# Performance work log

Measured on AMD Instinct MI355X. Metric: run time of the kernel, lower is better.

## Reference

```python
import math
import jax, jax.numpy as jnp
import numpy as np

B, N, C, H = 64, 197, 768, 12
KEEP_RATE = 0.7

def setup_inputs() -> dict:
    key = jax.random.key(0)
    k0, k1, k2 = jax.random.split(key, 3)
    x = jax.random.normal(k0, (B, N, C), jnp.float32)
    qkv_w = jax.random.normal(k1, (C, 3 * C), jnp.float32) * 0.02
    qkv_b = jnp.zeros((3 * C,), jnp.float32)
    proj_w = jax.random.normal(k2, (C, C), jnp.float32) * 0.02
    proj_b = jnp.zeros((C,), jnp.float32)
    return {"x": x, "qkv_w": qkv_w, "qkv_b": qkv_b, "proj_w": proj_w, "proj_b": proj_b}

def reference(x, qkv_w, qkv_b, proj_w, proj_b):
    b, n, c = x.shape
    d = c // H
    scale = d ** -0.5
    # qkv: [B,N,3C] -> [3,B,H,N,d]
    qkv = (x @ qkv_w + qkv_b).reshape(b, n, 3, H, d)
    qkv = jnp.transpose(qkv, (2, 0, 3, 1, 4))
    q, k, v = qkv[0], qkv[1], qkv[2]
    attn = jax.nn.softmax(jnp.einsum('bhnd,bhmd->bhnm', q, k) * scale, axis=-1)  # [B,H,N,N]
    out = jnp.einsum('bhnm,bhmd->bhnd', attn, v)          # [B,H,N,d]
    out = jnp.transpose(out, (0, 2, 1, 3)).reshape(b, n, c)
    x_out = out @ proj_w + proj_b                          # [B,N,C]
    # dynamic token pruning via CLS attention (row 0, excluding CLS itself)
    left_tokens = math.ceil(KEEP_RATE * (n - 1))
    cls_attn = attn[:, :, 0, 1:].mean(axis=1)              # [B,N-1]
    _, idx = jax.lax.top_k(cls_attn, left_tokens)          # descending, sorted
    index = jnp.broadcast_to(idx[:, :, None], (b, left_tokens, c))
    return (x_out, index, idx, cls_attn, left_tokens)
```

## Files before the change

### kernel.cpp

```cpp
#include <hip/hip_runtime.h>
#include <math.h>

#define BB   64
#define NTOK 197
#define CC   768
#define HH   12
#define DH   64
#define MTOT (BB * NTOK)
#define MPAD 12672
#define LEFT 138

#define XOUT_OFF  0
#define INDEX_OFF 9682944
#define IDX_OFF   16465920
#define CLS_OFF   16474752
#define LT_OFF    16487296

typedef short s8v __attribute__((ext_vector_type(8)));
typedef short s4v __attribute__((ext_vector_type(4)));
typedef float f4v __attribute__((ext_vector_type(4)));

#define GLOAD16(g, l) __builtin_amdgcn_global_load_lds( \
    (const __attribute__((address_space(1))) unsigned int*)(g), \
    (__attribute__((address_space(3))) unsigned int*)(l), 16, 0, 0)

__device__ __forceinline__ unsigned short f2bf(float f) {
    union { float f; unsigned int i; } x; x.f = f;
    unsigned int r = x.i + 0x7FFFu + ((x.i >> 16) & 1u);
    return (unsigned short)(r >> 16);
}


__device__ __forceinline__ void convert_x_body(int blk, int tid,
        const float* __restrict__ in, unsigned short* __restrict__ outb)
{
    size_t i = ((size_t)blk * 256 + tid) * 8;
    float4 a = *(const float4*)(in + i);
    float4 b = *(const float4*)(in + i + 4);
    s8v r;
    r[0] = (short)f2bf(a.x); r[1] = (short)f2bf(a.y);
    r[2] = (short)f2bf(a.z); r[3] = (short)f2bf(a.w);
    r[4] = (short)f2bf(b.x); r[5] = (short)f2bf(b.y);
    r[6] = (short)f2bf(b.z); r[7] = (short)f2bf(b.w);
    *(s8v*)(outb + i) = r;
}

__device__ __forceinline__ void transpose_w_body(int q, int tid, char* smem,
        const float* __restrict__ inq, const float* __restrict__ inp,
        unsigned short* __restrict__ outq, unsigned short* __restrict__ outp)
{
    float (*tile)[33] = (float(*)[33])smem;
    const int bi = q % 24;
    int bj = q / 24;
    const float* in; unsigned short* outb; int N;
    if (bj < 72) { in = inq; outb = outq; N = 2304; }
    else         { bj -= 72; in = inp; outb = outp; N = 768; }
    const int tx = tid & 31, ty = tid >> 5;
#pragma unroll
    for (int r = ty; r < 32; r += 8)
        tile[r][tx] = in[(size_t)(bi * 32 + r) * N + bj * 32 + tx];
    __syncthreads();
#pragma unroll
    for (int r = ty; r < 32; r += 8)
        outb[(size_t)(bj * 32 + r) * 768 + bi * 32 + tx] = f2bf(tile[tx][r]);
}

#define QCH  64
#define BGRP 8
__device__ __forceinline__ void qr96_body(int q, int tid, char* smem,
        const float* __restrict__ x, const float* __restrict__ qkv_w,
        const float* __restrict__ qkv_b, float* __restrict__ rws,
        float* __restrict__ bconst)
{
    const int h  = q % HH;
    const int b0 = (q / HH) * BGRP;
    float (*x0s)[CC] = (float(*)[CC])smem;
    float* wbuf0 = (float*)(smem + 24576);
    float* wbuf1 = (float*)(smem + 40960);
    float (*q0s)[DH] = (float(*)[DH])(smem + 57344);

    for (int u = tid; u < BGRP * CC; u += 256) {
        int b = u / CC, c = u - b * CC;
        x0s[b][c] = x[(size_t)(b0 + b) * NTOK * CC + c];
    }
    for (int u = tid; u < QCH * DH; u += 256) {
        int cc = u >> 6, dd = u & 63;
        wbuf0[u] = qkv_w[(size_t)cc * 2304 + h * DH + dd];
    }
    __syncthreads();

    const int d  = tid & 63;
    const int bA = tid >> 6;
    const int bB = bA + 4;
    float accA = qkv_b[h * DH + d];
    float accB = qkv_b[h * DH + d];
    for (int k = 0; k < CC / QCH; ++k) {
        float* wcur  = (k & 1) ? wbuf1 : wbuf0;
        float* wnext = (k & 1) ? wbuf0 : wbuf1;
        if (k + 1 < CC / QCH) {
            const int cbase = (k + 1) * QCH;
            for (int u = tid; u < QCH * DH; u += 256) {
                int cc = u >> 6, dd = u & 63;
                wnext[u] = qkv_w[(size_t)(cbase + cc) * 2304 + h * DH + dd];
            }
        }
        const int cb = k * QCH;
#pragma unroll
        for (int cc = 0; cc < QCH; ++cc) {
            const float wv = wcur[cc * 64 + d];
            accA = fmaf(x0s[bA][cb + cc], wv, accA);
            accB = fmaf(x0s[bB][cb + cc], wv, accB);
        }
        __syncthreads();
    }
    q0s[bA][d] = accA;
    q0s[bB][d] = accB;
    __syncthreads();

    if (tid < BGRP) {
        float acc3 = 0.f;
        for (int dd = 0; dd < DH; ++dd) acc3 += q0s[tid][dd] * qkv_b[CC + h * DH + dd];
        bconst[(b0 + tid) * HH + h] = acc3;
    }

    for (int c = tid; c < CC; c += 256) {
        const float* wrow = qkv_w + (size_t)c * 2304 + CC + h * DH;
        float acc2[BGRP];
#pragma unroll
        for (int b = 0; b < BGRP; ++b) acc2[b] = 0.f;
#pragma unroll
        for (int dd = 0; dd < DH; dd += 4) {
            float4 w4 = *(const float4*)(wrow + dd);
#pragma unroll
            for (int b = 0; b < BGRP; ++b) {
                acc2[b] = fmaf(w4.x, q0s[b][dd + 0], acc2[b]);
                acc2[b] = fmaf(w4.y, q0s[b][dd + 1], acc2[b]);
                acc2[b] = fmaf(w4.z, q0s[b][dd + 2], acc2[b]);
                acc2[b] = fmaf(w4.w, q0s[b][dd + 3], acc2[b]);
            }
        }
#pragma unroll
        for (int b = 0; b < BGRP; ++b)
            rws[((size_t)(b0 + b) * HH + h) * CC + c] = acc2[b];
    }
}

__device__ __forceinline__ void gemm_body(int id, int tid, char* smem,
        const unsigned short* __restrict__ A, const unsigned short* __restrict__ BT,
        const float* __restrict__ bias, int ncolt, int mode,
        unsigned short* __restrict__ outb, float* __restrict__ outf)
{
    const int xcd = id & 7;
    const int t = id >> 3;
    const int ct = t % ncolt, s = t / ncolt;
    const int rt = s * 8 + xcd;
    if (rt >= 99) return;
    const int m0 = rt * 128, n0 = ct * 128;

    const int wave = tid >> 6, lane = tid & 63;
    const int quad = lane >> 4, l16 = lane & 15;
    const int rowbase = (wave >> 1) * 64, colbase = (wave & 1) * 64;
    short* As = (short*)smem;
    short* Bs = (short*)(smem + 16384);

    const int rA   = lane >> 3;
    const int gcol = ((lane & 7) ^ rA) * 8;
    unsigned int agof[4], bgof[4];
#pragma unroll
    for (int i = 0; i < 4; ++i) {
        int c = wave * 4 + i;
        agof[i] = (unsigned int)((m0 + c * 8 + rA) * 768 + gcol);
        bgof[i] = (unsigned int)((n0 + c * 8 + rA) * 768 + gcol);
    }
    int aoff[4], boff[4];
#pragma unroll
    for (int i = 0; i < 4; ++i) {
        aoff[i] = (rowbase + i * 16 + l16) * 64 + ((quad ^ (l16 & 7)) * 8);
        boff[i] = (colbase + i * 16 + l16) * 64 + ((quad ^ (l16 & 7)) * 8);
    }

    f4v acc[4][4];
#pragma unroll
    for (int i = 0; i < 4; ++i)
#pragma unroll
        for (int j = 0; j < 4; ++j) acc[i][j] = (f4v)0.f;

    for (int k0 = 0; k0 < 768; k0 += 64) {
#pragma unroll
        for (int i = 0; i < 4; ++i) {
            int c = wave * 4 + i;
            GLOAD16(A  + agof[i] + k0, &As[c * 512]);
            GLOAD16(BT + bgof[i] + k0, &Bs[c * 512]);
        }
        __syncthreads();
#pragma unroll
        for (int ks = 0; ks < 2; ++ks) {
            const int x = ks * 32;
            s8v af[4], bf[4];
#pragma unroll
            for (int i = 0; i < 4; ++i) af[i] = *(const s8v*)&As[aoff[i] ^ x];
#pragma unroll
            for (int j = 0; j < 4; ++j) bf[j] = *(const s8v*)&Bs[boff[j] ^ x];
#pragma unroll
            for (int i = 0; i < 4; ++i)
#pragma unroll
                for (int j = 0; j < 4; ++j)
                    acc[i][j] = __builtin_amdgcn_mfma_f32_16x16x32_bf16(bf[j], af[i], acc[i][j], 0, 0, 0);
        }
        __syncthreads();
    }

    const int ncols = mode ? 768 : 2304;
#pragma unroll
    for (int i = 0; i < 4; ++i) {
        const int m = m0 + rowbase + i * 16 + l16;
        if (m >= MTOT) continue;
#pragma unroll
        for (int j = 0; j < 4; ++j) {
            const int nb = n0 + colbase + j * 16 + quad * 4;
            float4 b4 = *(const float4*)&bias[nb];
            if (mode == 1) {
                float4 r;
                r.x = acc[i][j][0] + b4.x; r.y = acc[i][j][1] + b4.y;
                r.z = acc[i][j][2] + b4.z; r.w = acc[i][j][3] + b4.w;
                *(float4*)(outf + (size_t)m * ncols + nb) = r;
            } else {
                s4v r;
                r[0] = (short)f2bf(acc[i][j][0] + b4.x);
                r[1] = (short)f2bf(acc[i][j][1] + b4.y);
                r[2] = (short)f2bf(acc[i][j][2] + b4.z);
                r[3] = (short)f2bf(acc[i][j][3] + b4.w);
                *(s4v*)(outb + (size_t)m * ncols + nb) = r;
            }
        }
    }
}

__device__ __forceinline__ void cls_s_body(int q, int tid, char* smem,
        const float* __restrict__ x, const float* __restrict__ rws,
        const float* __restrict__ bconst, float* __restrict__ sws)
{
    const int bx = q % 10, b = q / 10;
    float* rl  = (float*)smem;
    float* bcs = (float*)(smem + 37056);
#pragma unroll
    for (int h = 0; h < HH; ++h)
        for (int c = tid; c < CC; c += 256)
            rl[h * 772 + c] = rws[((size_t)b * HH + h) * CC + c];
    if (tid < HH) bcs[tid] = bconst[b * HH + tid];
    __syncthreads();
    const int local = bx * 256 + tid;
    if (local < NTOK * HH) {
        const int tok = local / HH;
        const int h = local - tok * HH;
        const float* xr = x + ((size_t)b * NTOK + tok) * CC;
        const float* rp = rl + h * 772;
        float acc = 0.f;
#pragma unroll 8
        for (int c = 0; c < CC; c += 4) {
            float4 x4 = *(const float4*)(xr + c);
            float4 r4 = *(const float4*)(rp + c);
            acc = fmaf(x4.x, r4.x, acc);
            acc = fmaf(x4.y, r4.y, acc);
            acc = fmaf(x4.z, r4.z, acc);
            acc = fmaf(x4.w, r4.w, acc);
        }
        sws[((size_t)b * HH + h) * NTOK + tok] = (acc + bcs[h]) * 0.125f;
    }
}

#define VTS 224
__device__ __forceinline__ void transpose_v_body(int q, int tid, char* smem,
        const unsigned short* __restrict__ qkv, unsigned short* __restrict__ vt)
{
    short (*tile)[33] = (short(*)[33])smem;
    const int bx = q % 7;
    const int by = (q / 7) & 1;
    const int bh = q / 14;
    const int b = bh / HH, h = bh - b * HH;
    const int tx = tid & 31, ty = tid >> 5;
    const unsigned short* vin = qkv + (size_t)b * NTOK * 2304 + 1536 + h * DH;
#pragma unroll
    for (int r = ty; r < 32; r += 8) {
        const int tok = bx * 32 + r;
        tile[r][tx] = (tok < NTOK) ? (short)vin[(size_t)tok * 2304 + by * 32 + tx] : (short)0;
    }
    __syncthreads();
#pragma unroll
    for (int r = ty; r < 32; r += 8) {
        const int d = by * 32 + r;
        vt[((size_t)bh * DH + d) * VTS + bx * 32 + tx] = tile[tx][r];
    }
}

__device__ __forceinline__ void cls_topk_body(int b, int tid, char* smem,
        const float* __restrict__ sws, float* __restrict__ out, int write_lt)
{
    const int wave = tid >> 6, lane = tid & 63;
    float (*sbuf)[208] = (float(*)[208])smem;
    float (*pm)[208]   = (float(*)[208])(smem + 9984);
    float* vals        = (float*)(smem + 13312);
    int*   idxs        = (int*)(smem + 14336);

    for (int jj = lane; jj < 208; jj += 64) pm[wave][jj] = 0.f;
    if (tid < NTOK) {
#pragma unroll
        for (int h = 0; h < HH; ++h)
            sbuf[h][tid] = sws[((size_t)b * HH + h) * NTOK + tid];
    }
    __syncthreads();

    for (int h = wave; h < HH; h += 4) {
        float sv[4], ev[4];
        float mx = -1e30f;
#pragma unroll
        for (int t = 0; t < 4; ++t) {
            int j = lane + 64 * t;
            sv[t] = (j < NTOK) ? sbuf[h][j] : -1e30f;
            mx = fmaxf(mx, sv[t]);
        }
#pragma unroll
        for (int off = 1; off < 64; off <<= 1) mx = fmaxf(mx, __shfl_xor(mx, off, 64));
        float sm = 0.f;
#pragma unroll
        for (int t = 0; t < 4; ++t) {
            int j = lane + 64 * t;
            ev[t] = (j < NTOK) ? expf(sv[t] - mx) : 0.f;
            sm += ev[t];
        }
#pragma unroll
        for (int off = 1; off < 64; off <<= 1) sm += __shfl_xor(sm, off, 64);
#pragma unroll
        for (int t = 0; t < 4; ++t) {
            int j = lane + 64 * t;
            if (j < NTOK) pm[wave][j] += ev[t] / sm;
        }
    }
    __syncthreads();

    float v = -INFINITY;
    int id = 256 + tid;
    if (tid < NTOK - 1) {
        int j = tid + 1;
        float s = ((pm[0][j] + pm[1][j]) + (pm[2][j] + pm[3][j])) * (1.f / 12.f);
        v = s; id = tid;
        out[CLS_OFF + (size_t)b * (NTOK - 1) + tid] = s;
    }
    vals[tid] = v; idxs[tid] = id;
    __syncthreads();

    for (int k = 2; k <= 256; k <<= 1) {
        for (int j = k >> 1; j > 0; j >>= 1) {
            int ixj = tid ^ j;
            if (ixj > tid) {
                float va = vals[tid], vb2 = vals[ixj];
                int ia = idxs[tid], ib = idxs[ixj];
                bool aLess = (va > vb2) || (va == vb2 && ia < ib);
                bool dir = ((tid & k) == 0);
                if (dir != aLess) {
                    vals[tid] = vb2; vals[ixj] = va;
                    idxs[tid] = ib;  idxs[ixj] = ia;
                }
            }
            __syncthreads();
        }
    }

    if (tid < LEFT) out[IDX_OFF + (size_t)b * LEFT + tid] = (float)idxs[tid];
    if (write_lt && b == 0 && tid == 0) out[LT_OFF] = (float)LEFT;
}

__device__ __forceinline__ void write_index_body(int row, int tid,
        const float* __restrict__ idx_in, float* __restrict__ out)
{
    const float v = idx_in[row];
    if (tid < 192) {
        float4 r; r.x = v; r.y = v; r.z = v; r.w = v;
        *(float4*)(out + INDEX_OFF + (size_t)row * CC + tid * 4) = r;
    }
}

#define PSTR 226
__device__ __forceinline__ void attn_body(int bh, int g, int tid,
        short* Ks, short* Ps,
        const unsigned short* __restrict__ qkv, const unsigned short* __restrict__ vt,
        unsigned short* __restrict__ attnbf)
{
    const int b = bh / HH, h = bh - b * HH;
    const int wave = tid >> 6, lane = tid & 63;
    const int quad = lane >> 4, l16 = lane & 15;

    const unsigned short* qg = qkv + (size_t)b * NTOK * 2304 + h * DH;
    const unsigned short* kg = qg + 768;
    const unsigned short* vtb = vt + (size_t)bh * DH * VTS;

    for (int u = tid; u < NTOK * 8; u += 256) {
        const int row = u >> 3, seg = u & 7;
        *(s8v*)&Ks[row * 64 + (seg ^ (row & 7)) * 8] =
            *(const s8v*)(kg + (size_t)row * 2304 + seg * 8);
    }
    __syncthreads();

    const int strip = g * 4 + wave;
    if (strip >= 13) return;

    const int mq = min(strip * 16 + l16, NTOK - 1);
    const s8v aq0 = *(const s8v*)(qg + (size_t)mq * 2304 + quad * 8);
    const s8v aq1 = *(const s8v*)(qg + (size_t)mq * 2304 + 32 + quad * 8);

    f4v sacc[14];
#pragma unroll
    for (int j = 0; j < 14; ++j) sacc[j] = (f4v)0.f;
    __builtin_amdgcn_s_setprio(1);
#pragma unroll
    for (int j = 0; j < 14; ++j) {
        const int kt = min(j * 16 + l16, NTOK - 1);
        s8v bk0 = *(const s8v*)&Ks[kt * 64 + ((quad       ^ (kt & 7)) * 8)];
        s8v bk1 = *(const s8v*)&Ks[kt * 64 + (((quad + 4) ^ (kt & 7)) * 8)];
        sacc[j] = __builtin_amdgcn_mfma_f32_16x16x32_bf16(bk0, aq0, sacc[j], 0, 0, 0);
        sacc[j] = __builtin_amdgcn_mfma_f32_16x16x32_bf16(bk1, aq1, sacc[j], 0, 0, 0);
    }
    __builtin_amdgcn_s_setprio(0);

    s8v bvr[7][4];
#pragma unroll
    for (int t = 0; t < 7; ++t) {
        const int ko = t * 32 + quad * 8;
#pragma unroll
        for (int j = 0; j < 4; ++j)
            bvr[t][j] = *(const s8v*)(vtb + (size_t)(j * 16 + l16) * VTS + ko);
    }

    float mx = -1e30f;
#pragma unroll
    for (int j = 0; j < 14; ++j)
#pragma unroll
        for (int r = 0; r < 4; ++r) {
            const int key = j * 16 + quad * 4 + r;
            float s = (key < NTOK) ? sacc[j][r] * 0.125f : -1e30f;
            sacc[j][r] = s;
            mx = fmaxf(mx, s);
        }
    mx = fmaxf(mx, __shfl_xor(mx, 16, 64));
    mx = fmaxf(mx, __shfl_xor(mx, 32, 64));

    float sm = 0.f;
#pragma unroll
    for (int j = 0; j < 14; ++j) {
        s4v pk;
#pragma unroll
        for (int r = 0; r < 4; ++r) {
            const int key = j * 16 + quad * 4 + r;
            float p = (key < NTOK) ? __expf(sacc[j][r] - mx) : 0.f;
            sm += p;
            pk[r] = (short)f2bf(p);
        }
        *(s4v*)&Ps[wave * 16 * PSTR + l16 * PSTR + j * 16 + quad * 4] = pk;
    }
    sm += __shfl_xor(sm, 16, 64);
    sm += __shfl_xor(sm, 32, 64);
    const float rcp = 1.f / sm;

    f4v oacc[4];
#pragma unroll
    for (int j = 0; j < 4; ++j) oacc[j] = (f4v)0.f;
    __builtin_amdgcn_s_setprio(1);
#pragma unroll
    for (int t = 0; t < 7; ++t) {
        const int ko = t * 32 + quad * 8;
        s8v ap = *(const s8v*)&Ps[wave * 16 * PSTR + l16 * PSTR + ko];
#pragma unroll
        for (int j = 0; j < 4; ++j)
            oacc[j] = __builtin_amdgcn_mfma_f32_16x16x32_bf16(bvr[t][j], ap, oacc[j], 0, 0, 0);
    }
    __builtin_amdgcn_s_setprio(0);
    const int qrow = strip * 16 + l16;
    if (qrow < NTOK) {
#pragma unroll
        for (int j = 0; j < 4; ++j) {
            s4v o4;
#pragma unroll
            for (int r = 0; r < 4; ++r) o4[r] = (short)f2bf(oacc[j][r] * rcp);
            *(s4v*)&attnbf[((size_t)b * NTOK + qrow) * 768 + h * DH + j * 16 + quad * 4] = o4;
        }
    }
}

#define PRE_QR 96
#define PRE_CV 4728
#define PRE_TW 2304

__global__ __launch_bounds__(256)
void fat_pre(const float* __restrict__ x, const float* __restrict__ qkv_w,
             const float* __restrict__ qkv_b, const float* __restrict__ proj_w,
             unsigned short* __restrict__ xbf, unsigned short* __restrict__ wt1,
             unsigned short* __restrict__ wt2, float* __restrict__ rws,
             float* __restrict__ bconst)
{
    __shared__ __align__(16) char smem[59392];
    const int id = blockIdx.x, tid = threadIdx.x;
    if (id < PRE_QR)
        qr96_body(id, tid, smem, x, qkv_w, qkv_b, rws, bconst);
    else if (id < PRE_QR + PRE_CV)
        convert_x_body(id - PRE_QR, tid, x, xbf);
    else
        transpose_w_body(id - PRE_QR - PRE_CV, tid, smem, qkv_w, proj_w, wt1, wt2);
}

#define QKV_GEMM (8 * 18 * 13)

__global__ __launch_bounds__(256, 3)
void fat_qkv(const unsigned short* __restrict__ xbf, const unsigned short* __restrict__ wt1,
             const float* __restrict__ qkv_b, unsigned short* __restrict__ qkvbf,
             const float* __restrict__ x, const float* __restrict__ rws,
             const float* __restrict__ bconst, float* __restrict__ sws)
{
    __shared__ __align__(16) char smem[37104];
    const int id = blockIdx.x, tid = threadIdx.x;
    if (id < QKV_GEMM)
        gemm_body(id, tid, smem, xbf, wt1, qkv_b, 18, 0, qkvbf, nullptr);
    else
        cls_s_body(id - QKV_GEMM, tid, smem, x, rws, bconst, sws);
}

__global__ __launch_bounds__(256)
void fat_tv(const unsigned short* __restrict__ qkvbf, unsigned short* __restrict__ vt,
            const float* __restrict__ sws, float* __restrict__ out, int write_lt)
{
    __shared__ __align__(16) char smem[15360];
    const int id = blockIdx.x, tid = threadIdx.x;
    if (id < 64)
        cls_topk_body(id, tid, smem, sws, out, write_lt);
    else
        transpose_v_body(id - 64, tid, smem, qkvbf, vt);
}

#define ATTN_BLKS (768 * 4)

__global__ __launch_bounds__(256, 2)
void fat_attn(const unsigned short* __restrict__ qkv, const unsigned short* __restrict__ vt,
              unsigned short* __restrict__ attnbf,
              const float* __restrict__ idx_in, float* __restrict__ out)
{
    __shared__ __align__(16) short Ks[NTOK * 64];
    __shared__ short Ps[4 * 16 * PSTR];
    const int id = blockIdx.x, tid = threadIdx.x;
    if (id < ATTN_BLKS)
        attn_body(id % 768, id / 768, tid, Ks, Ps, qkv, vt, attnbf);
    else
        write_index_body(id - ATTN_BLKS, tid, idx_in, out);
}

#define PROJ_GEMM (8 * 6 * 13)

__global__ __launch_bounds__(256, 3)
void fat_proj(const unsigned short* __restrict__ atbf, const unsigned short* __restrict__ wt2,
              const float* __restrict__ proj_b, float* __restrict__ outf)
{
    __shared__ __align__(16) char smem[32768];
    gemm_body(blockIdx.x, threadIdx.x, smem, atbf, wt2, proj_b, 6, 1, nullptr, outf);
}

extern "C" void kernel_launch(void* const* d_in, const int* in_sizes, int n_in,
                              void* d_out, int out_size, void* d_ws, size_t ws_size,
                              hipStream_t stream)
{
    const float* x      = (const float*)d_in[0];
    const float* qkv_w  = (const float*)d_in[1];
    const float* qkv_b  = (const float*)d_in[2];
    const float* proj_w = (const float*)d_in[3];
    const float* proj_b = (const float*)d_in[4];
    float* out = (float*)d_out;

    char* w = (char*)d_ws;
    unsigned short* xbf   = (unsigned short*)w; w += (size_t)MPAD * CC * 2;
    unsigned short* wt1   = (unsigned short*)w; w += (size_t)3 * CC * CC * 2;
    unsigned short* wt2   = (unsigned short*)w; w += (size_t)CC * CC * 2;
    unsigned short* qkvbf = (unsigned short*)w; w += (size_t)MTOT * 3 * CC * 2;
    unsigned short* atbf  = (unsigned short*)w; w += (size_t)MPAD * CC * 2;
    float* rws    = (float*)w; w += (size_t)BB * HH * CC * 4;
    float* bconst = (float*)w; w += (size_t)BB * HH * 4;
    float* sws    = (float*)w; w += (size_t)BB * HH * NTOK * 4;
    unsigned short* vtbf  = (unsigned short*)d_ws;

    fat_pre<<<dim3(PRE_QR + PRE_CV + PRE_TW), 256, 0, stream>>>(
        x, qkv_w, qkv_b, proj_w, xbf, wt1, wt2, rws, bconst);
    fat_qkv<<<dim3(QKV_GEMM + 640), 256, 0, stream>>>(
        xbf, wt1, qkv_b, qkvbf, x, rws, bconst, sws);
    fat_tv<<<dim3(64 + 7 * 2 * BB * HH), 256, 0, stream>>>(
        qkvbf, vtbf, sws, out, (out_size > LT_OFF) ? 1 : 0);
    fat_attn<<<dim3(ATTN_BLKS + BB * LEFT), 256, 0, stream>>>(
        qkvbf, vtbf, atbf, out + IDX_OFF, out);
    fat_proj<<<dim3(PROJ_GEMM), 256, 0, stream>>>(atbf, wt2, proj_b, out + XOUT_OFF);
}
```

Baseline: 334.6 us.

## Move index writes into proj kernel, shrink qr96 LDS, raise occupancy bounds

Splits attention back into a standalone 2D-grid kernel and moves the broadcast index write blocks into the projection GEMM launch. The qr96 block no longer stages weights through double-buffered LDS; it reads qkv_w directly from global memory, which cuts fat_pre shared memory from about 58KB to 26KB. Launch bounds for the qkv and proj kernels are raised from 3 to 4 blocks per SM to allow more resident waves. Possible downsides are extra register pressure and uncoalesced or repeated global weight loads in qr96.

```diff
diff --git a/kernel.cpp b/kernel.cpp
--- a/kernel.cpp
+++ b/kernel.cpp
@@ -65,7 +65,6 @@
         outb[(size_t)(bj * 32 + r) * 768 + bi * 32 + tx] = f2bf(tile[tx][r]);
 }
 
-#define QCH  64
 #define BGRP 8
 __device__ __forceinline__ void qr96_body(int q, int tid, char* smem,
         const float* __restrict__ x, const float* __restrict__ qkv_w,
@@ -75,17 +74,11 @@
     const int h  = q % HH;
     const int b0 = (q / HH) * BGRP;
     float (*x0s)[CC] = (float(*)[CC])smem;
-    float* wbuf0 = (float*)(smem + 24576);
-    float* wbuf1 = (float*)(smem + 40960);
-    float (*q0s)[DH] = (float(*)[DH])(smem + 57344);
+    float (*q0s)[DH] = (float(*)[DH])(smem + 24576);
 
     for (int u = tid; u < BGRP * CC; u += 256) {
         int b = u / CC, c = u - b * CC;
         x0s[b][c] = x[(size_t)(b0 + b) * NTOK * CC + c];
-    }
-    for (int u = tid; u < QCH * DH; u += 256) {
-        int cc = u >> 6, dd = u & 63;
-        wbuf0[u] = qkv_w[(size_t)cc * 2304 + h * DH + dd];
     }
     __syncthreads();
 
@@ -94,24 +87,11 @@
     const int bB = bA + 4;
     float accA = qkv_b[h * DH + d];
     float accB = qkv_b[h * DH + d];
-    for (int k = 0; k < CC / QCH; ++k) {
-        float* wcur  = (k & 1) ? wbuf1 : wbuf0;
-        float* wnext = (k & 1) ? wbuf0 : wbuf1;
-        if (k + 1 < CC / QCH) {
-            const int cbase = (k + 1) * QCH;
-            for (int u = tid; u < QCH * DH; u += 256) {
-                int cc = u >> 6, dd = u & 63;
-                wnext[u] = qkv_w[(size_t)(cbase + cc) * 2304 + h * DH + dd];
-            }
-        }
-        const int cb = k * QCH;
-#pragma unroll
-        for (int cc = 0; cc < QCH; ++cc) {
-            const float wv = wcur[cc * 64 + d];
-            accA = fmaf(x0s[bA][cb + cc], wv, accA);
-            accB = fmaf(x0s[bB][cb + cc], wv, accB);
-        }
-        __syncthreads();
+#pragma unroll 8
+    for (int c = 0; c < CC; ++c) {
+        const float wv = qkv_w[(size_t)c * 2304 + h * DH + d];
+        accA = fmaf(x0s[bA][c], wv, accA);
+        accB = fmaf(x0s[bB][c], wv, accB);
     }
     q0s[bA][d] = accA;
     q0s[bB][d] = accB;
@@ -380,112 +360,6 @@
     }
 }
 
-#define PSTR 226
-__device__ __forceinline__ void attn_body(int bh, int g, int tid,
-        short* Ks, short* Ps,
-        const unsigned short* __restrict__ qkv, const unsigned short* __restrict__ vt,
-        unsigned short* __restrict__ attnbf)
-{
-    const int b = bh / HH, h = bh - b * HH;
-    const int wave = tid >> 6, lane = tid & 63;
-    const int quad = lane >> 4, l16 = lane & 15;
-
-    const unsigned short* qg = qkv + (size_t)b * NTOK * 2304 + h * DH;
-    const unsigned short* kg = qg + 768;
-    const unsigned short* vtb = vt + (size_t)bh * DH * VTS;
-
-    for (int u = tid; u < NTOK * 8; u += 256) {
-        const int row = u >> 3, seg = u & 7;
-        *(s8v*)&Ks[row * 64 + (seg ^ (row & 7)) * 8] =
-            *(const s8v*)(kg + (size_t)row * 2304 + seg * 8);
-    }
-    __syncthreads();
-
-    const int strip = g * 4 + wave;
-    if (strip >= 13) return;
-
-    const int mq = min(strip * 16 + l16, NTOK - 1);
-    const s8v aq0 = *(const s8v*)(qg + (size_t)mq * 2304 + quad * 8);
-    const s8v aq1 = *(const s8v*)(qg + (size_t)mq * 2304 + 32 + quad * 8);
-
-    f4v sacc[14];
-#pragma unroll
-    for (int j = 0; j < 14; ++j) sacc[j] = (f4v)0.f;
-    __builtin_amdgcn_s_setprio(1);
-#pragma unroll
-    for (int j = 0; j < 14; ++j) {
-        const int kt = min(j * 16 + l16, NTOK - 1);
-        s8v bk0 = *(const s8v*)&Ks[kt * 64 + ((quad       ^ (kt & 7)) * 8)];
-        s8v bk1 = *(const s8v*)&Ks[kt * 64 + (((quad + 4) ^ (kt & 7)) * 8)];
-        sacc[j] = __builtin_amdgcn_mfma_f32_16x16x32_bf16(bk0, aq0, sacc[j], 0, 0, 0);
-        sacc[j] = __builtin_amdgcn_mfma_f32_16x16x32_bf16(bk1, aq1, sacc[j], 0, 0, 0);
-    }
-    __builtin_amdgcn_s_setprio(0);
-
-    s8v bvr[7][4];
-#pragma unroll
-    for (int t = 0; t < 7; ++t) {
-        const int ko = t * 32 + quad * 8;
-#pragma unroll
-        for (int j = 0; j < 4; ++j)
-            bvr[t][j] = *(const s8v*)(vtb + (size_t)(j * 16 + l16) * VTS + ko);
-    }
-
-    float mx = -1e30f;
-#pragma unroll
-    for (int j = 0; j < 14; ++j)
-#pragma unroll
-        for (int r = 0; r < 4; ++r) {
-            const int key = j * 16 + quad * 4 + r;
-            float s = (key < NTOK) ? sacc[j][r] * 0.125f : -1e30f;
-            sacc[j][r] = s;
-            mx = fmaxf(mx, s);
-        }
-    mx = fmaxf(mx, __shfl_xor(mx, 16, 64));
-    mx = fmaxf(mx, __shfl_xor(mx, 32, 64));
-
-    float sm = 0.f;
-#pragma unroll
-    for (int j = 0; j < 14; ++j) {
-        s4v pk;
-#pragma unroll
-        for (int r = 0; r < 4; ++r) {
-            const int key = j * 16 + quad * 4 + r;
-            float p = (key < NTOK) ? __expf(sacc[j][r] - mx) : 0.f;
-            sm += p;
-            pk[r] = (short)f2bf(p);
-        }
-        *(s4v*)&Ps[wave * 16 * PSTR + l16 * PSTR + j * 16 + quad * 4] = pk;
-    }
-    sm += __shfl_xor(sm, 16, 64);
-    sm += __shfl_xor(sm, 32, 64);
-    const float rcp = 1.f / sm;
-
-    f4v oacc[4];
-#pragma unroll
-    for (int j = 0; j < 4; ++j) oacc[j] = (f4v)0.f;
-    __builtin_amdgcn_s_setprio(1);
-#pragma unroll
-    for (int t = 0; t < 7; ++t) {
-        const int ko = t * 32 + quad * 8;
-        s8v ap = *(const s8v*)&Ps[wave * 16 * PSTR + l16 * PSTR + ko];
-#pragma unroll
-        for (int j = 0; j < 4; ++j)
-            oacc[j] = __builtin_amdgcn_mfma_f32_16x16x32_bf16(bvr[t][j], ap, oacc[j], 0, 0, 0);
-    }
-    __builtin_amdgcn_s_setprio(0);
-    const int qrow = strip * 16 + l16;
-    if (qrow < NTOK) {
-#pragma unroll
-        for (int j = 0; j < 4; ++j) {
-            s4v o4;
-#pragma unroll
-            for (int r = 0; r < 4; ++r) o4[r] = (short)f2bf(oacc[j][r] * rcp);
-            *(s4v*)&attnbf[((size_t)b * NTOK + qrow) * 768 + h * DH + j * 16 + quad * 4] = o4;
-        }
-    }
-}
-
 #define PRE_QR 96
 #define PRE_CV 4728
 #define PRE_TW 2304
@@ -497,7 +371,7 @@
              unsigned short* __restrict__ wt2, float* __restrict__ rws,
              float* __restrict__ bconst)
 {
-    __shared__ __align__(16) char smem[59392];
+    __shared__ __align__(16) char smem[26624];
     const int id = blockIdx.x, tid = threadIdx.x;
     if (id < PRE_QR)
         qr96_body(id, tid, smem, x, qkv_w, qkv_b, rws, bconst);
@@ -509,7 +383,7 @@
 
 #define QKV_GEMM (8 * 18 * 13)
 
-__global__ __launch_bounds__(256, 3)
+__global__ __launch_bounds__(256, 4)
 void fat_qkv(const unsigned short* __restrict__ xbf, const unsigned short* __restrict__ wt1,
              const float* __restrict__ qkv_b, unsigned short* __restrict__ qkvbf,
              const float* __restrict__ x, const float* __restrict__ rws,
@@ -535,30 +409,130 @@
         transpose_v_body(id - 64, tid, smem, qkvbf, vt);
 }
 
-#define ATTN_BLKS (768 * 4)
+#define PSTR 226
 
 __global__ __launch_bounds__(256, 2)
-void fat_attn(const unsigned short* __restrict__ qkv, const unsigned short* __restrict__ vt,
-              unsigned short* __restrict__ attnbf,
+void attn_mfma4(const unsigned short* __restrict__ qkv, const unsigned short* __restrict__ vt,
+                unsigned short* __restrict__ attnbf)
+{
+    const int bh = blockIdx.x;
+    const int g  = blockIdx.y;
+    const int b = bh / HH, h = bh - b * HH;
+    const int tid = threadIdx.x;
+    const int wave = tid >> 6, lane = tid & 63;
+    const int quad = lane >> 4, l16 = lane & 15;
+    __shared__ __align__(16) short Ks[NTOK * 64];
+    __shared__ short Ps[4][16 * PSTR];
+
+    const unsigned short* qg = qkv + (size_t)b * NTOK * 2304 + h * DH;
+    const unsigned short* kg = qg + 768;
+    const unsigned short* vtb = vt + (size_t)bh * DH * VTS;
+
+    for (int u = tid; u < NTOK * 8; u += 256) {
+        const int row = u >> 3, seg = u & 7;
+        *(s8v*)&Ks[row * 64 + (seg ^ (row & 7)) * 8] =
+            *(const s8v*)(kg + (size_t)row * 2304 + seg * 8);
+    }
+    __syncthreads();
+
+    const int strip = g * 4 + wave;
+    if (strip >= 13) return;
+
+    const int mq = min(strip * 16 + l16, NTOK - 1);
+    const s8v aq0 = *(const s8v*)(qg + (size_t)mq * 2304 + quad * 8);
+    const s8v aq1 = *(const s8v*)(qg + (size_t)mq * 2304 + 32 + quad * 8);
+
+    f4v sacc[14];
+#pragma unroll
+    for (int j = 0; j < 14; ++j) sacc[j] = (f4v)0.f;
+    __builtin_amdgcn_s_setprio(1);
+#pragma unroll
+    for (int j = 0; j < 14; ++j) {
+        const int kt = min(j * 16 + l16, NTOK - 1);
+        s8v bk0 = *(const s8v*)&Ks[kt * 64 + ((quad       ^ (kt & 7)) * 8)];
+        s8v bk1 = *(const s8v*)&Ks[kt * 64 + (((quad + 4) ^ (kt & 7)) * 8)];
+        sacc[j] = __builtin_amdgcn_mfma_f32_16x16x32_bf16(bk0, aq0, sacc[j], 0, 0, 0);
+        sacc[j] = __builtin_amdgcn_mfma_f32_16x16x32_bf16(bk1, aq1, sacc[j], 0, 0, 0);
+    }
+    __builtin_amdgcn_s_setprio(0);
+
+    s8v bvr[7][4];
+#pragma unroll
+    for (int t = 0; t < 7; ++t) {
+        const int ko = t * 32 + quad * 8;
+#pragma unroll
+        for (int j = 0; j < 4; ++j)
+            bvr[t][j] = *(const s8v*)(vtb + (size_t)(j * 16 + l16) * VTS + ko);
+    }
+
+    float mx = -1e30f;
+#pragma unroll
+    for (int j = 0; j < 14; ++j)
+#pragma unroll
+        for (int r = 0; r < 4; ++r) {
+            const int key = j * 16 + quad * 4 + r;
+            float s = (key < NTOK) ? sacc[j][r] * 0.125f : -1e30f;
+            sacc[j][r] = s;
+            mx = fmaxf(mx, s);
+        }
+    mx = fmaxf(mx, __shfl_xor(mx, 16, 64));
+    mx = fmaxf(mx, __shfl_xor(mx, 32, 64));
+
+    float sm = 0.f;
+#pragma unroll
+    for (int j = 0; j < 14; ++j) {
+        s4v pk;
+#pragma unroll
+        for (int r = 0; r < 4; ++r) {
+            const int key = j * 16 + quad * 4 + r;
+            float p = (key < NTOK) ? __expf(sacc[j][r] - mx) : 0.f;
+            sm += p;
+            pk[r] = (short)f2bf(p);
+        }
+        *(s4v*)&Ps[wave][l16 * PSTR + j * 16 + quad * 4] = pk;
+    }
+    sm += __shfl_xor(sm, 16, 64);
+    sm += __shfl_xor(sm, 32, 64);
+    const float rcp = 1.f / sm;
+
+    f4v oacc[4];
+#pragma unroll
+    for (int j = 0; j < 4; ++j) oacc[j] = (f4v)0.f;
+    __builtin_amdgcn_s_setprio(1);
+#pragma unroll
+    for (int t = 0; t < 7; ++t) {
+        const int ko = t * 32 + quad * 8;
+        s8v ap = *(const s8v*)&Ps[wave][l16 * PSTR + ko];
+#pragma unroll
+        for (int j = 0; j < 4; ++j)
+            oacc[j] = __builtin_amdgcn_mfma_f32_16x16x32_bf16(bvr[t][j], ap, oacc[j], 0, 0, 0);
+    }
+    __builtin_amdgcn_s_setprio(0);
+    const int qrow = strip * 16 + l16;
+    if (qrow < NTOK) {
+#pragma unroll
+        for (int j = 0; j < 4; ++j) {
+            s4v o4;
+#pragma unroll
+            for (int r = 0; r < 4; ++r) o4[r] = (short)f2bf(oacc[j][r] * rcp);
+            *(s4v*)&attnbf[((size_t)b * NTOK + qrow) * 768 + h * DH + j * 16 + quad * 4] = o4;
+        }
+    }
+}
+
+#define PROJ_GEMM (8 * 6 * 13)
+
+__global__ __launch_bounds__(256, 4)
+void fat_proj(const unsigned short* __restrict__ atbf, const unsigned short* __restrict__ wt2,
+              const float* __restrict__ proj_b, float* __restrict__ outf,
               const float* __restrict__ idx_in, float* __restrict__ out)
 {
-    __shared__ __align__(16) short Ks[NTOK * 64];
-    __shared__ short Ps[4 * 16 * PSTR];
+    __shared__ __align__(16) char smem[32768];
     const int id = blockIdx.x, tid = threadIdx.x;
-    if (id < ATTN_BLKS)
-        attn_body(id % 768, id / 768, tid, Ks, Ps, qkv, vt, attnbf);
+    if (id < PROJ_GEMM)
+        gemm_body(id, tid, smem, atbf, wt2, proj_b, 6, 1, nullptr, outf);
     else
-        write_index_body(id - ATTN_BLKS, tid, idx_in, out);
-}
-
-#define PROJ_GEMM (8 * 6 * 13)
-
-__global__ __launch_bounds__(256, 3)
-void fat_proj(const unsigned short* __restrict__ atbf, const unsigned short* __restrict__ wt2,
-              const float* __restrict__ proj_b, float* __restrict__ outf)
-{
-    __shared__ __align__(16) char smem[32768];
-    gemm_body(blockIdx.x, threadIdx.x, smem, atbf, wt2, proj_b, 6, 1, nullptr, outf);
+        write_index_body(id - PROJ_GEMM, tid, idx_in, out);
 }
 
 extern "C" void kernel_launch(void* const* d_in, const int* in_sizes, int n_in,
@@ -589,7 +563,7 @@
         xbf, wt1, qkv_b, qkvbf, x, rws, bconst, sws);
     fat_tv<<<dim3(64 + 7 * 2 * BB * HH), 256, 0, stream>>>(
         qkvbf, vtbf, sws, out, (out_size > LT_OFF) ? 1 : 0);
-    fat_attn<<<dim3(ATTN_BLKS + BB * LEFT), 256, 0, stream>>>(
-        qkvbf, vtbf, atbf, out + IDX_OFF, out);
-    fat_proj<<<dim3(PROJ_GEMM), 256, 0, stream>>>(atbf, wt2, proj_b, out + XOUT_OFF);
-}
+    attn_mfma4<<<dim3(BB * HH, 4), 256, 0, stream>>>(qkvbf, vtbf, atbf);
+    fat_proj<<<dim3(PROJ_GEMM + BB * LEFT), 256, 0, stream>>>(
+        atbf, wt2, proj_b, out + XOUT_OFF, out + IDX_OFF, out);
+}
```

After: 320.1 us. 1.05x faster.
